# Kernel tuning notes

Measured on AMD Instinct MI355X. Metric: run time of the kernel, lower is better.

## Reference

```python
import jax, jax.numpy as jnp
from jax import lax
import numpy as np

UNITS = 256
H = W = 64
INPUT_DIM = 128
FLAT = 64 * (H - 3) * (W - 3)  # conv stack output after same-conv, valid-conv, 2x2 avgpool stride 1


def setup_inputs() -> dict:
    key = jax.random.key(0)
    ks = jax.random.split(key, 8)
    s = lambda k, shape, fan: jax.random.normal(k, shape, jnp.float32) / np.sqrt(fan)
    return {
        "inputs": jax.random.normal(ks[0], (1, INPUT_DIM), jnp.float32),
        "memory": jax.random.normal(ks[1], (H * W, UNITS), jnp.float32),
        "conv_kernel1": s(ks[2], (3, 3, UNITS, 32), 9 * UNITS),
        "conv_kernel2": s(ks[3], (3, 3, 32, 64), 9 * 32),
        "conv_dense1": s(ks[4], (FLAT, 128), FLAT),
        "conv_dense2": s(ks[5], (128, UNITS), 128),
        "context_kernel": s(ks[6], (INPUT_DIM + UNITS, UNITS), INPUT_DIM + UNITS),
        "recurr_kernel": s(ks[7], (INPUT_DIM + UNITS, UNITS), UNITS),
        "x": 32,
        "y": 17,
    }


def reference(inputs, memory, conv_kernel1, conv_kernel2, conv_dense1,
              conv_dense2, context_kernel, recurrent_kernel=None, recurr_kernel=None,
              x=32, y=17):
    rec = recurr_kernel if recurr_kernel is not None else recurrent_kernel
    input_dim = inputs.shape[-1]
    # memory: (H*W, units) -> (1, units, H, W)  (channels_first)
    mem = memory.T.reshape(1, UNITS, H, W)
    dn = ("NCHW", "HWIO", "NCHW")
    c1 = lax.conv_general_dilated(mem, conv_kernel1, (1, 1), "SAME", dimension_numbers=dn)   # (1,32,H,W)
    c2 = lax.conv_general_dilated(c1, conv_kernel2, (1, 1), "VALID", dimension_numbers=dn)   # (1,64,H-2,W-2)
    pool = lax.reduce_window(c2, 0.0, lax.add, (1, 1, 2, 2), (1, 1, 1, 1), "VALID") * 0.25   # (1,64,H-3,W-3)
    flat = pool.reshape(1, -1)
    r_t = (flat @ conv_dense1) @ conv_dense2                      # (1, units)
    q_t = jnp.concatenate([inputs, r_t], axis=-1) @ context_kernel  # (1, units)
    m = mem[0]                                                    # (units, H, W)
    m2 = m.reshape(UNITS, H * W)
    scores = q_t @ m2                                             # (1, H*W)
    at = jax.nn.softmax(scores, axis=-1)                          # softmax over all positions
    c_t = at @ m2.T                                               # (1, units) attention read
    write_kernel = rec[:input_dim]
    write_update = rec[input_dim:]
    s_t = inputs @ write_kernel                                   # (1, units)
    global_imp = jnp.sum(s_t * r_t)
    local_imp = jnp.sum(s_t * c_t)
    mem_t = m[:, x, y][None, :]                                   # gather single slot (1, units)
    mem_t = mem_t + local_imp / (local_imp + global_imp) * ((mem_t - s_t) @ write_update)
    new_mem = m.at[:, x, y].set(mem_t[0])                         # scatter slot back
    return c_t, r_t, new_mem
```

## Files before the change

### kernel.cpp

```cpp
#include <hip/hip_runtime.h>

#define FLAT  238144
#define NB_R1 931

#define W_C2   0
#define W_P1   246016
#define W_RT   365184
#define W_ST   365440
#define W_QT   365696
#define W_QTA  365952
#define W_STAT 366208
#define W_PC   366336
#define W_WARM 382720
#define W_END  382736

#define F_C2   140416
#define F_P1   386432
#define F_RT   505600
#define F_ST   505856
#define F_QT   506112
#define F_QTA  506368
#define F_STAT 510464
#define F_PC   510592

__device__ __forceinline__ int read_idx(const int* p) {
    unsigned int u = (unsigned int)*p;
    int ex = (int)((u >> 23) & 0xFF);
    int v;
    if (ex >= 118 && ex <= 140) {
        union { unsigned int i; float f; } c; c.i = u;
        v = (int)(c.f + 0.5f);
    } else {
        v = (int)u;
    }
    return v < 0 ? 0 : (v > 63 ? 63 : v);
}

__global__ __launch_bounds__(256) void k_conv1(const float* __restrict__ mem,
                                               const float* __restrict__ k1,
                                               float* __restrict__ c1p) {
    __shared__ float sm[32 * 105];
    __shared__ __align__(16) float sk[9 * 32 * 32];
    int t = threadIdx.x;
    int th = (blockIdx.x >> 3) * 8;
    int tw = (blockIdx.x & 7) * 8;
    int chunk = blockIdx.y;
    {
        float4 mv[4];
        #pragma unroll
        for (int k = 0; k < 4; ++k) {
            int u = t + k * 256;
            float4 v = make_float4(0.f, 0.f, 0.f, 0.f);
            if (u < 800) {
                int pix = u >> 3, c4 = u & 7;
                int hh = th - 1 + pix / 10;
                int ww = tw - 1 + pix % 10;
                if ((unsigned)hh < 64u && (unsigned)ww < 64u)
                    v = *(const float4*)(mem + (size_t)(hh * 64 + ww) * 256
                                             + chunk * 32 + c4 * 4);
            }
            mv[k] = v;
        }
        #pragma unroll
        for (int k = 0; k < 4; ++k) {
            int u = t + k * 256;
            if (u < 800) {
                int pix = u >> 3, c4 = u & 7;
                int ib = c4 * 4;
                sm[(ib    ) * 105 + pix] = mv[k].x;
                sm[(ib + 1) * 105 + pix] = mv[k].y;
                sm[(ib + 2) * 105 + pix] = mv[k].z;
                sm[(ib + 3) * 105 + pix] = mv[k].w;
            }
        }
    }
    {
        float4 kv[9];
        #pragma unroll
        for (int k = 0; k < 9; ++k)
            kv[k] = ((const float4*)(k1 + (size_t)k * 8192
                                        + (size_t)chunk * 1024))[t];
        #pragma unroll
        for (int k = 0; k < 9; ++k)
            *(float4*)&sk[k * 1024 + t * 4] = kv[k];
    }
    __syncthreads();
    int lh = (t & 63) >> 3, lw = t & 7, og = t >> 6;
    float acc[8];
    #pragma unroll
    for (int j = 0; j < 8; ++j) acc[j] = 0.f;
    for (int dh = 0; dh < 3; ++dh)
        for (int dw = 0; dw < 3; ++dw) {
            int pixb = (lh + dh) * 10 + (lw + dw);
            const float* kt = sk + (dh * 3 + dw) * 1024 + og * 8;
            #pragma unroll 4
            for (int i = 0; i < 32; ++i) {
                float m = sm[i * 105 + pixb];
                float4 ka = *(const float4*)(kt + i * 32);
                float4 kb = *(const float4*)(kt + i * 32 + 4);
                acc[0] += m * ka.x; acc[1] += m * ka.y;
                acc[2] += m * ka.z; acc[3] += m * ka.w;
                acc[4] += m * kb.x; acc[5] += m * kb.y;
                acc[6] += m * kb.z; acc[7] += m * kb.w;
            }
        }
    int p = (th + lh) * 64 + tw + lw;
    float* dst = c1p + (size_t)chunk * 131072 + (size_t)(og * 8) * 4096 + p;
    #pragma unroll
    for (int j = 0; j < 8; ++j)
        dst[(size_t)j * 4096] = acc[j];
}

__global__ __launch_bounds__(256) void k_c1red(float* __restrict__ c1p) {
    int idx = blockIdx.x * 256 + threadIdx.x;
    float s = 0.f;
    #pragma unroll
    for (int c = 0; c < 8; ++c) s += c1p[(size_t)c * 131072 + idx];
    c1p[idx] = s;
}

__global__ __launch_bounds__(256) void k_conv2(const float* __restrict__ c1p,
                                               const float* __restrict__ k2,
                                               float* __restrict__ c2,
                                               int nchunks) {
    __shared__ float sm[32 * 104];
    __shared__ __align__(16) float sk2[9 * 32 * 16];
    int t = threadIdx.x;
    int th = (blockIdx.x >> 3) * 8;
    int tw = (blockIdx.x & 7) * 8;
    int o0 = blockIdx.y * 16;
    if (nchunks == 8) {
        #pragma unroll 2
        for (int u = t; u < 3200; u += 256) {
            int i = u / 100;
            int pix = u % 100;
            int hh = th + pix / 10;
            int ww = tw + pix % 10;
            float v = 0.f;
            if (hh < 64 && ww < 64) {
                const float* p = c1p + (size_t)i * 4096 + hh * 64 + ww;
                float a0 = p[0];
                float a1 = p[131072];
                float a2 = p[2 * 131072];
                float a3 = p[3 * 131072];
                float a4 = p[4 * 131072];
                float a5 = p[5 * 131072];
                float a6 = p[6 * 131072];
                float a7 = p[7 * 131072];
                v = a0 + a1 + a2 + a3 + a4 + a5 + a6 + a7;
            }
            sm[i * 104 + pix] = v;
        }
    } else {
        for (int u = t; u < 3200; u += 256) {
            int i = u / 100;
            int pix = u % 100;
            int hh = th + pix / 10;
            int ww = tw + pix % 10;
            float v = 0.f;
            if (hh < 64 && ww < 64)
                v = c1p[(size_t)i * 4096 + hh * 64 + ww];
            sm[i * 104 + pix] = v;
        }
    }
    {
        float4 kv[5];
        #pragma unroll
        for (int k = 0; k < 5; ++k) {
            int u = t + k * 256;
            if (u < 1152) {
                int tap = u >> 7, r = u & 127;
                int i = r >> 2, o4 = r & 3;
                kv[k] = *(const float4*)(k2 + (size_t)tap * 2048 + i * 64
                                            + o0 + o4 * 4);
            }
        }
        #pragma unroll
        for (int k = 0; k < 5; ++k) {
            int u = t + k * 256;
            if (u < 1152) {
                int tap = u >> 7, r = u & 127;
                int i = r >> 2, o4 = r & 3;
                *(float4*)&sk2[tap * 512 + i * 16 + o4 * 4] = kv[k];
            }
        }
    }
    __syncthreads();
    int pix = t & 63;
    int lh = pix >> 3, lw = pix & 7, og = t >> 6;
    float acc[4] = {0.f, 0.f, 0.f, 0.f};
    for (int dh = 0; dh < 3; ++dh)
        for (int dw = 0; dw < 3; ++dw) {
            int pixb = (lh + dh) * 10 + (lw + dw);
            const float* kt = sk2 + (dh * 3 + dw) * 512 + og * 4;
            #pragma unroll 8
            for (int i = 0; i < 32; ++i) {
                float m = sm[i * 104 + pixb];
                float4 kv = *(const float4*)(kt + i * 16);
                acc[0] += m * kv.x; acc[1] += m * kv.y;
                acc[2] += m * kv.z; acc[3] += m * kv.w;
            }
        }
    int h = th + lh, w = tw + lw;
    if (h < 62 && w < 62) {
        #pragma unroll
        for (int j = 0; j < 4; ++j)
            c2[(size_t)(o0 + og * 4 + j) * 3844 + h * 62 + w] = acc[j];
    }
}

__global__ __launch_bounds__(256) void k_r1pt(const float* __restrict__ c2,
                                              const float* __restrict__ d1,
                                              float* __restrict__ p1,
                                              const float* __restrict__ mem,
                                              const int* __restrict__ px,
                                              const int* __restrict__ py,
                                              float* __restrict__ outm,
                                              const float* __restrict__ d2,
                                              const float* __restrict__ ck,
                                              const float* __restrict__ rec,
                                              const float* __restrict__ inp,
                                              float* __restrict__ st,
                                              float* __restrict__ qta,
                                              float* __restrict__ warm,
                                              int withx) {
    __shared__ __align__(16) float SM[4160];
    int t = threadIdx.x;
    int bid = blockIdx.x;
    int fb = -1;
    if (!withx) {
        fb = bid;
    } else if (bid < 256) {
        int tu = bid;
        float* tile = SM;
        int p0 = (tu & 63) * 64;
        int u0 = (tu >> 6) * 64;
        int x = read_idx(px), y = read_idx(py);
        int pxy = x * 64 + y;
        int lane = t & 63, grp = t >> 6;
        for (int r = 0; r < 16; ++r) {
            int pr = grp + r * 4;
            tile[pr * 65 + lane] = mem[(size_t)(p0 + pr) * 256 + u0 + lane];
        }
        __syncthreads();
        for (int r = 0; r < 16; ++r) {
            int ur = grp + r * 4;
            if (p0 + lane != pxy)
                outm[(size_t)(u0 + ur) * 4096 + p0 + lane] = tile[lane * 65 + ur];
        }
        return;
    } else if (bid < 256 + NB_R1) {
        fb = bid - 256;
    } else if (bid == 256 + NB_R1) {
        float sv = 0.f;
        #pragma unroll 16
        for (int k = 0; k < 128; ++k) sv += inp[k] * rec[k * 256 + t];
        st[t] = sv;
        return;
    } else if (bid == 257 + NB_R1) {
        float q = 0.f;
        #pragma unroll 16
        for (int k = 0; k < 128; ++k) q += inp[k] * ck[k * 256 + t];
        qta[t] = q;
        return;
    } else {
        int wu = bid - (258 + NB_R1);
        float a = 0.f;
        for (int k = 0; k < 12; ++k) {
            int j = (wu * 256 + t) + k * 3584;
            if (j < 40960) {
                float4 v;
                if (j < 8192)        v = ((const float4*)d2 )[j];
                else if (j < 24576)  v = ((const float4*)rec)[j];
                else                 v = ((const float4*)ck )[j - 16384];
                a += v.x + v.y + v.z + v.w;
            }
        }
        SM[t] = a;
        __syncthreads();
        if (t == 0) {
            float s = 0.f;
            for (int i = 0; i < 256; ++i) s += SM[i];
            warm[wu] = s;
        }
        return;
    }
    {
        float* pl   = SM;
        float* sred = SM + 256;
        int f0 = fb * 256;
        int fmax = FLAT - f0; if (fmax > 256) fmax = 256;
        for (int s = t; s < fmax; s += 256) {
            int f = f0 + s;
            int o = f / 3721;
            int r = f % 3721;
            int h = r / 61, w = r % 61;
            const float* b = c2 + (size_t)o * 3844 + h * 62 + w;
            pl[s] = 0.25f * (b[0] + b[1] + b[62] + b[63]);
        }
        __syncthreads();
        int jq = t & 31, g = t >> 5;
        float4 a = make_float4(0.f, 0.f, 0.f, 0.f);
        if (fmax == 256) {
            #pragma unroll 8
            for (int it = 0; it < 32; ++it) {
                int s = g + it * 8;
                float m = pl[s];
                float4 dv = *(const float4*)(d1 + (size_t)(f0 + s) * 128 + jq * 4);
                a.x += m * dv.x; a.y += m * dv.y; a.z += m * dv.z; a.w += m * dv.w;
            }
        } else {
            for (int s = g; s < fmax; s += 8) {
                float m = pl[s];
                float4 dv = *(const float4*)(d1 + (size_t)(f0 + s) * 128 + jq * 4);
                a.x += m * dv.x; a.y += m * dv.y; a.z += m * dv.z; a.w += m * dv.w;
            }
        }
        *(float4*)&sred[(g * 32 + jq) * 4] = a;
        __syncthreads();
        if (t < 32) {
            float4 s4 = make_float4(0.f, 0.f, 0.f, 0.f);
            #pragma unroll
            for (int gg = 0; gg < 8; ++gg) {
                float4 v = *(const float4*)&sred[(gg * 32 + t) * 4];
                s4.x += v.x; s4.y += v.y; s4.z += v.z; s4.w += v.w;
            }
            *(float4*)(p1 + (size_t)fb * 128 + t * 4) = s4;
        }
    }
}

__global__ __launch_bounds__(1024) void k_fused(const float* __restrict__ p1,
                                                const float* __restrict__ d2,
                                                const float* __restrict__ inp,
                                                const float* __restrict__ ck,
                                                const float* __restrict__ rec,
                                                const float* __restrict__ qta,
                                                float* __restrict__ rt,
                                                float* __restrict__ qt,
                                                float* __restrict__ st,
                                                int haveAux) {
    __shared__ float p2s[8][128];
    __shared__ float s_r1[128], s_in[128], s_rt[256];
    int t = threadIdx.x;
    int j = t & 127, part = t >> 7;
    int b0 = part * 117;
    int b1 = b0 + 117; if (b1 > NB_R1) b1 = NB_R1;
    float s = 0.f;
    #pragma unroll 8
    for (int b = b0; b < b1; ++b) s += p1[b * 128 + j];
    p2s[part][j] = s;
    if (t < 128) s_in[t] = inp[t];
    __syncthreads();
    if (t < 128) {
        float r = 0.f;
        #pragma unroll
        for (int c = 0; c < 8; ++c) r += p2s[c][t];
        s_r1[t] = r;
    }
    __syncthreads();
    if (t < 256) {
        float a = 0.f;
        #pragma unroll 16
        for (int k = 0; k < 128; ++k) a += s_r1[k] * d2[k * 256 + t];
        rt[t] = a; s_rt[t] = a;
        if (!haveAux) {
            float sv = 0.f;
            #pragma unroll 16
            for (int k = 0; k < 128; ++k) sv += s_in[k] * rec[k * 256 + t];
            st[t] = sv;
        }
    }
    __syncthreads();
    if (t < 256) {
        float q;
        if (haveAux) {
            q = qta[t];
        } else {
            q = 0.f;
            #pragma unroll 16
            for (int k = 0; k < 128; ++k) q += s_in[k] * ck[k * 256 + t];
        }
        #pragma unroll 16
        for (int k = 0; k < 256; ++k) q += s_rt[k] * ck[(128 + k) * 256 + t];
        qt[t] = q;
    }
}

__global__ __launch_bounds__(256) void k_scores(const float* __restrict__ qt,
                                                const float* __restrict__ mem,
                                                float* __restrict__ stat,
                                                float* __restrict__ pc) {
    __shared__ float q[256];
    __shared__ float rowv[64], aL[64];
    __shared__ float mbS;
    int t = threadIdx.x;
    int bid = blockIdx.x;
    q[t] = qt[t];
    __syncthreads();
    int wave = t >> 6, lane = t & 63;
    float qx = q[lane * 4], qy = q[lane * 4 + 1],
          qz = q[lane * 4 + 2], qw = q[lane * 4 + 3];
    int p0 = bid * 64;
    for (int r = 0; r < 16; ++r) {
        int p = p0 + wave * 16 + r;
        float4 m = *(const float4*)(mem + (size_t)p * 256 + lane * 4);
        float acc = m.x * qx + m.y * qy + m.z * qz + m.w * qw;
        for (int off = 32; off; off >>= 1) acc += __shfl_down(acc, off);
        if (lane == 0) rowv[wave * 16 + r] = acc;
    }
    __syncthreads();
    if (t == 0) {
        float mb = rowv[0];
        for (int i = 1; i < 64; ++i) mb = fmaxf(mb, rowv[i]);
        mbS = mb;
    }
    __syncthreads();
    if (t < 64) aL[t] = expf(rowv[t] - mbS);
    __syncthreads();
    if (t == 0) {
        float sb = 0.f;
        for (int i = 0; i < 64; ++i) sb += aL[i];
        stat[bid * 2]     = mbS;
        stat[bid * 2 + 1] = sb;
    }
    float acc = 0.f;
    #pragma unroll 16
    for (int pp = 0; pp < 64; ++pp)
        acc += aL[pp] * mem[(size_t)(p0 + pp) * 256 + t];
    pc[bid * 256 + t] = acc;
}

__global__ __launch_bounds__(256) void k_final(const float* __restrict__ rt,
                                               const float* __restrict__ st,
                                               const float* __restrict__ stat,
                                               const float* __restrict__ pc,
                                               const float* __restrict__ mem,
                                               const float* __restrict__ rec,
                                               const int* __restrict__ px,
                                               const int* __restrict__ py,
                                               float* __restrict__ out) {
    __shared__ float s_diff[256], red[256];
    __shared__ float sm_[64], wb[64], aux[2];
    int t = threadIdx.x;
    int x = read_idx(px), y = read_idx(py);
    int pxy = x * 64 + y;
    if (t < 64) sm_[t] = stat[t * 2];
    __syncthreads();
    if (t == 0) {
        float M = sm_[0];
        for (int i = 1; i < 64; ++i) M = fmaxf(M, sm_[i]);
        float S = 0.f;
        for (int i = 0; i < 64; ++i) S += stat[i * 2 + 1] * expf(sm_[i] - M);
        aux[0] = M; aux[1] = 1.f / S;
    }
    __syncthreads();
    if (t < 64) wb[t] = expf(sm_[t] - aux[0]) * aux[1];
    __syncthreads();
    float ctv = 0.f;
    #pragma unroll 16
    for (int b = 0; b < 64; ++b) ctv += pc[b * 256 + t] * wb[b];
    float stv = st[t], rtv = rt[t];
    float memt = mem[(size_t)pxy * 256 + t];
    red[t] = stv * rtv; __syncthreads();
    for (int s = 128; s; s >>= 1) { if (t < s) red[t] += red[t + s]; __syncthreads(); }
    float gimp = red[0]; __syncthreads();
    red[t] = stv * ctv; __syncthreads();
    for (int s = 128; s; s >>= 1) { if (t < s) red[t] += red[t + s]; __syncthreads(); }
    float limp = red[0];
    s_diff[t] = memt - stv;
    __syncthreads();
    float d = 0.f;
    #pragma unroll 16
    for (int k = 0; k < 256; ++k)
        d += s_diff[k] * rec[(128 + k) * 256 + t];
    float frac = limp / (limp + gimp);
    out[t] = ctv;
    out[256 + t] = rtv;
    out[512 + (size_t)t * 4096 + pxy] = memt + frac * d;
}

__global__ __launch_bounds__(256) void k_transpose(const float* __restrict__ mem,
                                                   const int* __restrict__ px,
                                                   const int* __restrict__ py,
                                                   float* __restrict__ outm) {
    __shared__ float tile[64][65];
    int t = threadIdx.x;
    int p0 = blockIdx.x * 64;
    int u0 = blockIdx.y * 64;
    int x = read_idx(px), y = read_idx(py);
    int pxy = x * 64 + y;
    int lane = t & 63, grp = t >> 6;
    for (int r = 0; r < 16; ++r) {
        int pr = grp + r * 4;
        tile[pr][lane] = mem[(size_t)(p0 + pr) * 256 + u0 + lane];
    }
    __syncthreads();
    for (int r = 0; r < 16; ++r) {
        int ur = grp + r * 4;
        if (p0 + lane != pxy)
            outm[(size_t)(u0 + ur) * 4096 + p0 + lane] = tile[lane][ur];
    }
}

extern "C" void kernel_launch(void* const* d_in, const int* in_sizes, int n_in,
                              void* d_out, int out_size, void* d_ws, size_t ws_size,
                              hipStream_t stream) {
    const float* inp = (const float*)d_in[0];
    const float* mem = (const float*)d_in[1];
    const float* k1  = (const float*)d_in[2];
    const float* k2  = (const float*)d_in[3];
    const float* d1  = (const float*)d_in[4];
    const float* d2  = (const float*)d_in[5];
    const float* ck  = (const float*)d_in[6];
    const float* rec = (const float*)d_in[7];
    const int* px = (const int*)d_in[8];
    const int* py = (const int*)d_in[9];
    float* out = (float*)d_out;
    float* scr = out + 512;
    float* ws  = (float*)d_ws;

    bool useWs = (ws != nullptr) && (ws_size >= (size_t)W_END * sizeof(float));

    if (useWs) {
        k_conv1<<<dim3(64, 8), 256, 0, stream>>>(mem, k1, scr);
        k_conv2<<<dim3(64, 4), 256, 0, stream>>>(scr, k2, ws + W_C2, 8);
        k_r1pt<<<256 + NB_R1 + 16, 256, 0, stream>>>(
            ws + W_C2, d1, ws + W_P1, mem, px, py, scr,
            d2, ck, rec, inp, ws + W_ST, ws + W_QTA, ws + W_WARM, 1);
        k_fused<<<1, 1024, 0, stream>>>(ws + W_P1, d2, inp, ck, rec,
                                        ws + W_QTA, ws + W_RT, ws + W_QT,
                                        ws + W_ST, 1);
        k_scores<<<64, 256, 0, stream>>>(ws + W_QT, mem, ws + W_STAT,
                                         ws + W_PC);
        k_final<<<1, 256, 0, stream>>>(ws + W_RT, ws + W_ST, ws + W_STAT,
                                       ws + W_PC, mem, rec, px, py, out);
    } else {
        k_conv1<<<dim3(64, 8), 256, 0, stream>>>(mem, k1, scr);
        k_c1red<<<512, 256, 0, stream>>>(scr);
        k_conv2<<<dim3(64, 4), 256, 0, stream>>>(scr, k2, scr + F_C2, 1);
        k_r1pt<<<NB_R1, 256, 0, stream>>>(
            scr + F_C2, d1, scr + F_P1, mem, px, py, scr,
            d2, ck, rec, inp, scr + F_ST, scr + F_QTA, scr + F_PC + 16384, 0);
        k_fused<<<1, 1024, 0, stream>>>(scr + F_P1, d2, inp, ck, rec,
                                        scr + F_QTA, scr + F_RT, scr + F_QT,
                                        scr + F_ST, 0);
        k_scores<<<64, 256, 0, stream>>>(scr + F_QT, mem, scr + F_STAT,
                                         scr + F_PC);
        k_final<<<1, 256, 0, stream>>>(scr + F_RT, scr + F_ST, scr + F_STAT,
                                       scr + F_PC, mem, rec, px, py, out);
        k_transpose<<<dim3(64, 4), 256, 0, stream>>>(mem, px, py, out + 512);
    }
}
```

Before: 280.2 us.

## Move independent side work into conv1 kernel and give conv1 partials their own workspace

Renames conv1 to k_front and, in workspace mode, adds extra blocks that do the memory transpose copy, the s_t and q_t partial matvecs and the cache-warming reads, so these run alongside conv1 instead of alongside the dense reduction. The dense-reduction kernel is trimmed back to pooling plus the matmul with d1. Conv1 partial outputs now go to a separate workspace region instead of the output scratch. This means the transpose writes into scr and the conv1 partials no longer overlap in memory. The aim is better overlap and less contention in the bandwidth-bound d1 stage, at the cost of a larger workspace requirement.

```diff
diff --git a/kernel.cpp b/kernel.cpp
--- a/kernel.cpp
+++ b/kernel.cpp
@@ -12,7 +12,8 @@
 #define W_STAT 366208
 #define W_PC   366336
 #define W_WARM 382720
-#define W_END  382736
+#define W_C1P  382736
+#define W_END  1431312
 
 #define F_C2   140416
 #define F_P1   386432
@@ -36,15 +37,81 @@
     return v < 0 ? 0 : (v > 63 ? 63 : v);
 }
 
-__global__ __launch_bounds__(256) void k_conv1(const float* __restrict__ mem,
+__global__ __launch_bounds__(256) void k_front(const float* __restrict__ mem,
                                                const float* __restrict__ k1,
-                                               float* __restrict__ c1p) {
-    __shared__ float sm[32 * 105];
-    __shared__ __align__(16) float sk[9 * 32 * 32];
-    int t = threadIdx.x;
-    int th = (blockIdx.x >> 3) * 8;
-    int tw = (blockIdx.x & 7) * 8;
-    int chunk = blockIdx.y;
+                                               float* __restrict__ c1p,
+                                               const int* __restrict__ px,
+                                               const int* __restrict__ py,
+                                               float* __restrict__ outm,
+                                               const float* __restrict__ inp,
+                                               const float* __restrict__ rec,
+                                               const float* __restrict__ ck,
+                                               const float* __restrict__ d2,
+                                               float* __restrict__ st,
+                                               float* __restrict__ qta,
+                                               float* __restrict__ warm,
+                                               int mode) {
+    __shared__ __align__(16) float SM[12576];
+    int t = threadIdx.x;
+    int bid = blockIdx.x;
+    if (mode == 1 && bid >= 512) {
+        if (bid < 768) {
+            int tu = bid - 512;
+            float* tile = SM;
+            int p0 = (tu & 63) * 64;
+            int u0 = (tu >> 6) * 64;
+            int x = read_idx(px), y = read_idx(py);
+            int pxy = x * 64 + y;
+            int lane = t & 63, grp = t >> 6;
+            for (int r = 0; r < 16; ++r) {
+                int pr = grp + r * 4;
+                tile[pr * 65 + lane] = mem[(size_t)(p0 + pr) * 256 + u0 + lane];
+            }
+            __syncthreads();
+            for (int r = 0; r < 16; ++r) {
+                int ur = grp + r * 4;
+                if (p0 + lane != pxy)
+                    outm[(size_t)(u0 + ur) * 4096 + p0 + lane] =
+                        tile[lane * 65 + ur];
+            }
+        } else if (bid == 768) {
+            float sv = 0.f;
+            #pragma unroll 16
+            for (int k = 0; k < 128; ++k) sv += inp[k] * rec[k * 256 + t];
+            st[t] = sv;
+        } else if (bid == 769) {
+            float q = 0.f;
+            #pragma unroll 16
+            for (int k = 0; k < 128; ++k) q += inp[k] * ck[k * 256 + t];
+            qta[t] = q;
+        } else {
+            int wu = bid - 770;
+            float a = 0.f;
+            for (int k = 0; k < 12; ++k) {
+                int j = (wu * 256 + t) + k * 3584;
+                if (j < 40960) {
+                    float4 v;
+                    if (j < 8192)        v = ((const float4*)d2 )[j];
+                    else if (j < 24576)  v = ((const float4*)rec)[j];
+                    else                 v = ((const float4*)ck )[j - 16384];
+                    a += v.x + v.y + v.z + v.w;
+                }
+            }
+            SM[t] = a;
+            __syncthreads();
+            if (t == 0) {
+                float s = 0.f;
+                for (int i = 0; i < 256; ++i) s += SM[i];
+                warm[wu] = s;
+            }
+        }
+        return;
+    }
+    float* sm = SM;
+    float* sk = SM + 3360;
+    int th = ((bid & 63) >> 3) * 8;
+    int tw = (bid & 7) * 8;
+    int chunk = bid >> 6;
     {
         float4 mv[4];
         #pragma unroll
@@ -209,124 +276,52 @@
     }
 }
 
-__global__ __launch_bounds__(256) void k_r1pt(const float* __restrict__ c2,
-                                              const float* __restrict__ d1,
-                                              float* __restrict__ p1,
-                                              const float* __restrict__ mem,
-                                              const int* __restrict__ px,
-                                              const int* __restrict__ py,
-                                              float* __restrict__ outm,
-                                              const float* __restrict__ d2,
-                                              const float* __restrict__ ck,
-                                              const float* __restrict__ rec,
-                                              const float* __restrict__ inp,
-                                              float* __restrict__ st,
-                                              float* __restrict__ qta,
-                                              float* __restrict__ warm,
-                                              int withx) {
+__global__ __launch_bounds__(256) void k_r1p(const float* __restrict__ c2,
+                                             const float* __restrict__ d1,
+                                             float* __restrict__ p1) {
     __shared__ __align__(16) float SM[4160];
     int t = threadIdx.x;
-    int bid = blockIdx.x;
-    int fb = -1;
-    if (!withx) {
-        fb = bid;
-    } else if (bid < 256) {
-        int tu = bid;
-        float* tile = SM;
-        int p0 = (tu & 63) * 64;
-        int u0 = (tu >> 6) * 64;
-        int x = read_idx(px), y = read_idx(py);
-        int pxy = x * 64 + y;
-        int lane = t & 63, grp = t >> 6;
-        for (int r = 0; r < 16; ++r) {
-            int pr = grp + r * 4;
-            tile[pr * 65 + lane] = mem[(size_t)(p0 + pr) * 256 + u0 + lane];
-        }
-        __syncthreads();
-        for (int r = 0; r < 16; ++r) {
-            int ur = grp + r * 4;
-            if (p0 + lane != pxy)
-                outm[(size_t)(u0 + ur) * 4096 + p0 + lane] = tile[lane * 65 + ur];
-        }
-        return;
-    } else if (bid < 256 + NB_R1) {
-        fb = bid - 256;
-    } else if (bid == 256 + NB_R1) {
-        float sv = 0.f;
+    int fb = blockIdx.x;
+    float* pl   = SM;
+    float* sred = SM + 256;
+    int f0 = fb * 256;
+    int fmax = FLAT - f0; if (fmax > 256) fmax = 256;
+    for (int s = t; s < fmax; s += 256) {
+        int f = f0 + s;
+        int o = f / 3721;
+        int r = f % 3721;
+        int h = r / 61, w = r % 61;
+        const float* b = c2 + (size_t)o * 3844 + h * 62 + w;
+        pl[s] = 0.25f * (b[0] + b[1] + b[62] + b[63]);
+    }
+    __syncthreads();
+    int jq = t & 31, g = t >> 5;
+    float4 a = make_float4(0.f, 0.f, 0.f, 0.f);
+    if (fmax == 256) {
         #pragma unroll 16
-        for (int k = 0; k < 128; ++k) sv += inp[k] * rec[k * 256 + t];
-        st[t] = sv;
-        return;
-    } else if (bid == 257 + NB_R1) {
-        float q = 0.f;
-        #pragma unroll 16
-        for (int k = 0; k < 128; ++k) q += inp[k] * ck[k * 256 + t];
-        qta[t] = q;
-        return;
+        for (int it = 0; it < 32; ++it) {
+            int s = g + it * 8;
+            float m = pl[s];
+            float4 dv = *(const float4*)(d1 + (size_t)(f0 + s) * 128 + jq * 4);
+            a.x += m * dv.x; a.y += m * dv.y; a.z += m * dv.z; a.w += m * dv.w;
+        }
     } else {
-        int wu = bid - (258 + NB_R1);
-        float a = 0.f;
-        for (int k = 0; k < 12; ++k) {
-            int j = (wu * 256 + t) + k * 3584;
-            if (j < 40960) {
-                float4 v;
-                if (j < 8192)        v = ((const float4*)d2 )[j];
-                else if (j < 24576)  v = ((const float4*)rec)[j];
-                else                 v = ((const float4*)ck )[j - 16384];
-                a += v.x + v.y + v.z + v.w;
-            }
-        }
-        SM[t] = a;
-        __syncthreads();
-        if (t == 0) {
-            float s = 0.f;
-            for (int i = 0; i < 256; ++i) s += SM[i];
-            warm[wu] = s;
-        }
-        return;
-    }
-    {
-        float* pl   = SM;
-        float* sred = SM + 256;
-        int f0 = fb * 256;
-        int fmax = FLAT - f0; if (fmax > 256) fmax = 256;
-        for (int s = t; s < fmax; s += 256) {
-            int f = f0 + s;
-            int o = f / 3721;
-            int r = f % 3721;
-            int h = r / 61, w = r % 61;
-            const float* b = c2 + (size_t)o * 3844 + h * 62 + w;
-            pl[s] = 0.25f * (b[0] + b[1] + b[62] + b[63]);
-        }
-        __syncthreads();
-        int jq = t & 31, g = t >> 5;
-        float4 a = make_float4(0.f, 0.f, 0.f, 0.f);
-        if (fmax == 256) {
-            #pragma unroll 8
-            for (int it = 0; it < 32; ++it) {
-                int s = g + it * 8;
-                float m = pl[s];
-                float4 dv = *(const float4*)(d1 + (size_t)(f0 + s) * 128 + jq * 4);
-                a.x += m * dv.x; a.y += m * dv.y; a.z += m * dv.z; a.w += m * dv.w;
-            }
-        } else {
-            for (int s = g; s < fmax; s += 8) {
-                float m = pl[s];
-                float4 dv = *(const float4*)(d1 + (size_t)(f0 + s) * 128 + jq * 4);
-                a.x += m * dv.x; a.y += m * dv.y; a.z += m * dv.z; a.w += m * dv.w;
-            }
-        }
-        *(float4*)&sred[(g * 32 + jq) * 4] = a;
-        __syncthreads();
-        if (t < 32) {
-            float4 s4 = make_float4(0.f, 0.f, 0.f, 0.f);
-            #pragma unroll
-            for (int gg = 0; gg < 8; ++gg) {
-                float4 v = *(const float4*)&sred[(gg * 32 + t) * 4];
-                s4.x += v.x; s4.y += v.y; s4.z += v.z; s4.w += v.w;
-            }
-            *(float4*)(p1 + (size_t)fb * 128 + t * 4) = s4;
-        }
+        for (int s = g; s < fmax; s += 8) {
+            float m = pl[s];
+            float4 dv = *(const float4*)(d1 + (size_t)(f0 + s) * 128 + jq * 4);
+            a.x += m * dv.x; a.y += m * dv.y; a.z += m * dv.z; a.w += m * dv.w;
+        }
+    }
+    *(float4*)&sred[(g * 32 + jq) * 4] = a;
+    __syncthreads();
+    if (t < 32) {
+        float4 s4 = make_float4(0.f, 0.f, 0.f, 0.f);
+        #pragma unroll
+        for (int gg = 0; gg < 8; ++gg) {
+            float4 v = *(const float4*)&sred[(gg * 32 + t) * 4];
+            s4.x += v.x; s4.y += v.y; s4.z += v.z; s4.w += v.w;
+        }
+        *(float4*)(p1 + (size_t)fb * 128 + t * 4) = s4;
     }
 }
 
@@ -523,11 +518,11 @@
     bool useWs = (ws != nullptr) && (ws_size >= (size_t)W_END * sizeof(float));
 
     if (useWs) {
-        k_conv1<<<dim3(64, 8), 256, 0, stream>>>(mem, k1, scr);
-        k_conv2<<<dim3(64, 4), 256, 0, stream>>>(scr, k2, ws + W_C2, 8);
-        k_r1pt<<<256 + NB_R1 + 16, 256, 0, stream>>>(
-            ws + W_C2, d1, ws + W_P1, mem, px, py, scr,
-            d2, ck, rec, inp, ws + W_ST, ws + W_QTA, ws + W_WARM, 1);
+        k_front<<<784, 256, 0, stream>>>(mem, k1, ws + W_C1P, px, py, scr,
+                                         inp, rec, ck, d2,
+                                         ws + W_ST, ws + W_QTA, ws + W_WARM, 1);
+        k_conv2<<<dim3(64, 4), 256, 0, stream>>>(ws + W_C1P, k2, ws + W_C2, 8);
+        k_r1p<<<NB_R1, 256, 0, stream>>>(ws + W_C2, d1, ws + W_P1);
         k_fused<<<1, 1024, 0, stream>>>(ws + W_P1, d2, inp, ck, rec,
                                         ws + W_QTA, ws + W_RT, ws + W_QT,
                                         ws + W_ST, 1);
@@ -536,12 +531,13 @@
         k_final<<<1, 256, 0, stream>>>(ws + W_RT, ws + W_ST, ws + W_STAT,
                                        ws + W_PC, mem, rec, px, py, out);
     } else {
-        k_conv1<<<dim3(64, 8), 256, 0, stream>>>(mem, k1, scr);
+        k_front<<<512, 256, 0, stream>>>(mem, k1, scr, px, py, scr,
+                                         inp, rec, ck, d2,
+                                         scr + F_ST, scr + F_QTA,
+                                         scr + F_PC + 16384, 0);
         k_c1red<<<512, 256, 0, stream>>>(scr);
         k_conv2<<<dim3(64, 4), 256, 0, stream>>>(scr, k2, scr + F_C2, 1);
-        k_r1pt<<<NB_R1, 256, 0, stream>>>(
-            scr + F_C2, d1, scr + F_P1, mem, px, py, scr,
-            d2, ck, rec, inp, scr + F_ST, scr + F_QTA, scr + F_PC + 16384, 0);
+        k_r1p<<<NB_R1, 256, 0, stream>>>(scr + F_C2, d1, scr + F_P1);
         k_fused<<<1, 1024, 0, stream>>>(scr + F_P1, d2, inp, ck, rec,
                                         scr + F_QTA, scr + F_RT, scr + F_QT,
                                         scr + F_ST, 0);
```

Measured after the change: 278.0 us. About the same (-0.8%).
